# Kernel tuning notes

Measured on AMD Instinct MI355X. Metric: run time of the kernel, lower is better.

## Reference

```python
import jax, jax.numpy as jnp
import numpy as np
from math import factorial

D = 2          # qudit dimension
L = 13         # number of qudits: state dim = D**L = 8192
J, K = 0, 1    # levels coupled by the gate
CUTOFF = 10    # Taylor truncation order
INDEX = set(range(13))


def _series(z, parity):
    # sum_{i=1..CUTOFF, i%2==parity} z**i / i!   (truncated exp split into even/odd parts)
    s = jnp.zeros((), dtype=jnp.complex64)
    for i in range(1, CUTOFF + 1):
        if i % 2 == parity:
            s = s + z ** i / factorial(i)
    return s


def _gate(theta):
    # single-qudit RX gate matrix, truncated-Taylor version matching the torch code
    z = (-0.5j) * theta.astype(jnp.complex64)
    odd = _series(z, 1)   # ~ -i sin(theta/2)
    even = _series(z, 0)  # ~ cos(theta/2) - 1
    M = jnp.eye(D, dtype=jnp.complex64)
    M = M.at[J, K].add(odd)
    M = M.at[K, J].add(odd)
    M = M.at[J, J].add(even)
    M = M.at[K, K].add(even)
    return M


def setup_inputs() -> dict:
    key = jax.random.key(0)
    k1, k2, k3 = jax.random.split(key, 3)
    dim = D ** L
    return {
        "x_real": jax.random.normal(k1, (dim, 64), dtype=jnp.float32),
        "x_imag": jax.random.normal(k2, (dim, 64), dtype=jnp.float32),
        "angle": jax.random.normal(k3, (L,), dtype=jnp.float32),
    }


def reference(x_real, x_imag, angle):
    x = x_real.astype(jnp.complex64) + 1j * x_imag.astype(jnp.complex64)
    eye = jnp.eye(D, dtype=jnp.complex64)
    U = jnp.eye(1, dtype=jnp.complex64)
    for i in range(L):  # fixed structural loop over qudits (13 iterations)
        M = _gate(angle[i]) if i in INDEX else eye
        U = jnp.kron(U, M)
    out = U @ x  # [D^L, B] complex64
    return jnp.stack([out.real, out.imag])  # [2, D^L, B] float32
```

## Files before the change

### kernel.cpp

```cpp
#include <hip/hip_runtime.h>

#define PLANE (8192 * 64)

__device__ __forceinline__ void gate_coeffs(float theta, float& a, float& s) {
    float t = 0.5f * theta;
    float u = t * t;
    s = t * (1.f + u * (-1.f/6.f + u * (1.f/120.f + u * (-1.f/5040.f + u * (1.f/362880.f)))));
    a = 1.f + u * (-0.5f + u * (1.f/24.f + u * (-1.f/720.f + u * (1.f/40320.f + u * (-1.f/3628800.f)))));
}

__device__ __forceinline__ void butterfly(float4& v0, float4& v1, float a, float s) {
    float4 n0, n1;
    n0.x = a * v0.x + s * v1.y;
    n0.y = a * v0.y - s * v1.x;
    n0.z = a * v0.z + s * v1.w;
    n0.w = a * v0.w - s * v1.z;
    n1.x = a * v1.x + s * v0.y;
    n1.y = a * v1.y - s * v0.x;
    n1.z = a * v1.z + s * v0.w;
    n1.w = a * v1.w - s * v0.z;
    v0 = n0; v1 = n1;
}

__global__ __launch_bounds__(256) void rx_low(const float* __restrict__ xr,
                                              const float* __restrict__ xi,
                                              const float* __restrict__ angle,
                                              float4* __restrict__ ws4) {
    __shared__ float4 l4[64 * 8];
    const int tid = threadIdx.x;
    const int g   = blockIdx.x >> 2;
    const int q   = blockIdx.x & 3;

    const float4* xr4 = (const float4*)xr;
    const float4* xi4 = (const float4*)xi;

    {
        int lr = tid >> 2, c4 = tid & 3;
        int ga = (g * 64 + lr) * 16 + q * 4 + c4;
        float4 re = xr4[ga];
        float4 im = xi4[ga];
        l4[lr * 8 + c4 * 2]     = make_float4(re.x, im.x, re.y, im.y);
        l4[lr * 8 + c4 * 2 + 1] = make_float4(re.z, im.z, re.w, im.w);
    }
    __syncthreads();

    #pragma unroll
    for (int b = 0; b < 6; ++b) {
        float a, s;
        gate_coeffs(angle[12 - b], a, s);
        int cp = tid & 7, rp = tid >> 3;
        int lo = ((rp >> b) << (b + 1)) | (rp & ((1 << b) - 1));
        int i0 = lo * 8 + cp;
        int i1 = i0 + (8 << b);
        float4 v0 = l4[i0], v1 = l4[i1];
        butterfly(v0, v1, a, s);
        l4[i0] = v0; l4[i1] = v1;
        __syncthreads();
    }

    #pragma unroll
    for (int k = 0; k < 2; ++k) {
        int j = tid + 256 * k;
        int m = j >> 3, cp = j & 7;
        ws4[(q * 8192 + m * 128 + g) * 8 + cp] = l4[j];
    }
}

__global__ __launch_bounds__(256) void rx_high(const float* __restrict__ angle,
                                               const float4* __restrict__ ws4,
                                               float* __restrict__ out) {
    __shared__ float4 l4[128 * 8];
    const int tid = threadIdx.x;
    const int g   = blockIdx.x >> 2;
    const int q   = blockIdx.x & 3;

    const float4* src = ws4 + (size_t)(q * 8192 + g * 128) * 8;
    typedef const __attribute__((address_space(1))) unsigned int* g32;
    typedef __attribute__((address_space(3))) unsigned int* l32;
    #pragma unroll
    for (int k = 0; k < 4; ++k) {
        int j = tid + 256 * k;
        __builtin_amdgcn_global_load_lds((g32)(src + j), (l32)(l4 + j), 16, 0, 0);
    }
    asm volatile("s_waitcnt vmcnt(0)" ::: "memory");
    __syncthreads();

    #pragma unroll
    for (int qq = 0; qq < 7; ++qq) {
        float a, s;
        gate_coeffs(angle[6 - qq], a, s);
        #pragma unroll
        for (int pp = 0; pp < 2; ++pp) {
            int p  = tid + 256 * pp;
            int cp = p & 7, hp = p >> 3;
            int h0 = ((hp >> qq) << (qq + 1)) | (hp & ((1 << qq) - 1));
            int i0 = h0 * 8 + cp;
            int i1 = i0 + (8 << qq);
            float4 v0 = l4[i0], v1 = l4[i1];
            butterfly(v0, v1, a, s);
            l4[i0] = v0; l4[i1] = v1;
        }
        __syncthreads();
    }

    float2* outre2 = (float2*)out;
    float2* outim2 = (float2*)(out + PLANE);
    #pragma unroll
    for (int k = 0; k < 4; ++k) {
        int j = tid + 256 * k;
        int h = j >> 3, cp = j & 7;
        float4 v = l4[j];
        int r  = g + 64 * h;
        int o2 = r * 32 + q * 8 + cp;
        outre2[o2] = make_float2(v.x, v.z);
        outim2[o2] = make_float2(v.y, v.w);
    }
}

extern "C" void kernel_launch(void* const* d_in, const int* in_sizes, int n_in,
                              void* d_out, int out_size, void* d_ws, size_t ws_size,
                              hipStream_t stream) {
    const float* xr    = (const float*)d_in[0];
    const float* xi    = (const float*)d_in[1];
    const float* angle = (const float*)d_in[2];
    float*  out = (float*)d_out;
    float4* ws4 = (float4*)d_ws;

    rx_low<<<512, 256, 0, stream>>>(xr, xi, angle, ws4);
    rx_high<<<256, 256, 0, stream>>>(angle, ws4, out);
}
```

Baseline: 14.20 us.

## Fuse butterfly stages in registers, swizzle LDS, and retile high kernel

Each thread now does two qubit stages per LDS round trip (a radix-4 step over four rows held in registers). This halves the number of shared-memory passes and barriers. Both kernels use XOR-swizzled LDS indexing to avoid bank conflicts, and gate coefficients are computed up front. Blocks shrink to 128 threads, and the workspace layout is retiled so rx_high uses 512 blocks and writes float4 output rows instead of float2. The swizzled intermediate layout adds index arithmetic and must agree exactly between the two kernels.

```diff
diff --git a/kernel.cpp b/kernel.cpp
--- a/kernel.cpp
+++ b/kernel.cpp
@@ -9,111 +9,184 @@
     a = 1.f + u * (-0.5f + u * (1.f/24.f + u * (-1.f/720.f + u * (1.f/40320.f + u * (-1.f/3628800.f)))));
 }
 
-__device__ __forceinline__ void butterfly(float4& v0, float4& v1, float a, float s) {
+__device__ __forceinline__ void bf(float4& v0, float4& v1, float a, float s) {
     float4 n0, n1;
-    n0.x = a * v0.x + s * v1.y;
-    n0.y = a * v0.y - s * v1.x;
-    n0.z = a * v0.z + s * v1.w;
-    n0.w = a * v0.w - s * v1.z;
-    n1.x = a * v1.x + s * v0.y;
-    n1.y = a * v1.y - s * v0.x;
-    n1.z = a * v1.z + s * v0.w;
-    n1.w = a * v1.w - s * v0.z;
+    n0.x = a * v0.x + s * v1.y;  n0.y = a * v0.y - s * v1.x;
+    n0.z = a * v0.z + s * v1.w;  n0.w = a * v0.w - s * v1.z;
+    n1.x = a * v1.x + s * v0.y;  n1.y = a * v1.y - s * v0.x;
+    n1.z = a * v1.z + s * v0.w;  n1.w = a * v1.w - s * v0.z;
     v0 = n0; v1 = n1;
 }
 
-__global__ __launch_bounds__(256) void rx_low(const float* __restrict__ xr,
+__device__ __forceinline__ int swzA(int row, int cp) {
+    return row * 8 + (cp ^ ((row ^ (row >> 3)) & 7));
+}
+__device__ __forceinline__ int sB(int h) { return (h ^ (h >> 2) ^ (h >> 4)) & 3; }
+__device__ __forceinline__ int swzB(int h, int cp) {
+    return h * 4 + (cp ^ sB(h));
+}
+
+__global__ __launch_bounds__(128) void rx_low(const float* __restrict__ xr,
                                               const float* __restrict__ xi,
                                               const float* __restrict__ angle,
                                               float4* __restrict__ ws4) {
-    __shared__ float4 l4[64 * 8];
-    const int tid = threadIdx.x;
-    const int g   = blockIdx.x >> 2;
-    const int q   = blockIdx.x & 3;
+    __shared__ float4 la[512];
+    const int t  = threadIdx.x;
+    const int g  = blockIdx.x >> 2;
+    const int qq = blockIdx.x & 3;
+
+    float a0,s0,a1,s1,a2,s2,a3,s3,a4,s4,a5,s5;
+    gate_coeffs(angle[12], a0, s0);
+    gate_coeffs(angle[11], a1, s1);
+    gate_coeffs(angle[10], a2, s2);
+    gate_coeffs(angle[9],  a3, s3);
+    gate_coeffs(angle[8],  a4, s4);
+    gate_coeffs(angle[7],  a5, s5);
 
     const float4* xr4 = (const float4*)xr;
     const float4* xi4 = (const float4*)xi;
 
-    {
-        int lr = tid >> 2, c4 = tid & 3;
-        int ga = (g * 64 + lr) * 16 + q * 4 + c4;
-        float4 re = xr4[ga];
-        float4 im = xi4[ga];
-        l4[lr * 8 + c4 * 2]     = make_float4(re.x, im.x, re.y, im.y);
-        l4[lr * 8 + c4 * 2 + 1] = make_float4(re.z, im.z, re.w, im.w);
-    }
-    __syncthreads();
-
-    #pragma unroll
-    for (int b = 0; b < 6; ++b) {
-        float a, s;
-        gate_coeffs(angle[12 - b], a, s);
-        int cp = tid & 7, rp = tid >> 3;
-        int lo = ((rp >> b) << (b + 1)) | (rp & ((1 << b) - 1));
-        int i0 = lo * 8 + cp;
-        int i1 = i0 + (8 << b);
-        float4 v0 = l4[i0], v1 = l4[i1];
-        butterfly(v0, v1, a, s);
-        l4[i0] = v0; l4[i1] = v1;
-        __syncthreads();
-    }
-
     #pragma unroll
     for (int k = 0; k < 2; ++k) {
-        int j = tid + 256 * k;
-        int m = j >> 3, cp = j & 7;
-        ws4[(q * 8192 + m * 128 + g) * 8 + cp] = l4[j];
-    }
-}
-
-__global__ __launch_bounds__(256) void rx_high(const float* __restrict__ angle,
+        int j   = t + 128 * k;
+        int row = j >> 2, f4 = j & 3;
+        int ga  = (g * 64 + row) * 16 + qq * 4 + f4;
+        float4 re = xr4[ga], im = xi4[ga];
+        la[swzA(row, 2 * f4)]     = make_float4(re.x, im.x, re.y, im.y);
+        la[swzA(row, 2 * f4 + 1)] = make_float4(re.z, im.z, re.w, im.w);
+    }
+    __syncthreads();
+
+    const int cp = t & 7, grp = t >> 3;
+
+    {
+        int r0 = grp * 4;
+        float4 v0 = la[swzA(r0 + 0, cp)], v1 = la[swzA(r0 + 1, cp)];
+        float4 v2 = la[swzA(r0 + 2, cp)], v3 = la[swzA(r0 + 3, cp)];
+        bf(v0, v1, a0, s0); bf(v2, v3, a0, s0);
+        bf(v0, v2, a1, s1); bf(v1, v3, a1, s1);
+        la[swzA(r0 + 0, cp)] = v0; la[swzA(r0 + 1, cp)] = v1;
+        la[swzA(r0 + 2, cp)] = v2; la[swzA(r0 + 3, cp)] = v3;
+    }
+    __syncthreads();
+    {
+        int base = ((grp >> 2) << 4) | (grp & 3);
+        int r0 = base, r1 = base + 4, r2 = base + 8, r3 = base + 12;
+        float4 v0 = la[swzA(r0, cp)], v1 = la[swzA(r1, cp)];
+        float4 v2 = la[swzA(r2, cp)], v3 = la[swzA(r3, cp)];
+        bf(v0, v1, a2, s2); bf(v2, v3, a2, s2);
+        bf(v0, v2, a3, s3); bf(v1, v3, a3, s3);
+        la[swzA(r0, cp)] = v0; la[swzA(r1, cp)] = v1;
+        la[swzA(r2, cp)] = v2; la[swzA(r3, cp)] = v3;
+    }
+    __syncthreads();
+    {
+        int r0 = grp, r1 = grp + 16, r2 = grp + 32, r3 = grp + 48;
+        float4 v0 = la[swzA(r0, cp)], v1 = la[swzA(r1, cp)];
+        float4 v2 = la[swzA(r2, cp)], v3 = la[swzA(r3, cp)];
+        bf(v0, v1, a4, s4); bf(v2, v3, a4, s4);
+        bf(v0, v2, a5, s5); bf(v1, v3, a5, s5);
+        la[swzA(r0, cp)] = v0; la[swzA(r1, cp)] = v1;
+        la[swzA(r2, cp)] = v2; la[swzA(r3, cp)] = v3;
+    }
+    __syncthreads();
+
+    const int sbg = sB(g);
+    #pragma unroll
+    for (int k = 0; k < 4; ++k) {
+        int j  = t + 128 * k;
+        int m  = j >> 3, cp8 = j & 7;
+        int q  = qq * 2 + (cp8 >> 2), cb = cp8 & 3;
+        ws4[(q * 64 + m) * 512 + g * 4 + (cb ^ sbg)] = la[swzA(m, cp8)];
+    }
+}
+
+__global__ __launch_bounds__(128) void rx_high(const float* __restrict__ angle,
                                                const float4* __restrict__ ws4,
                                                float* __restrict__ out) {
-    __shared__ float4 l4[128 * 8];
-    const int tid = threadIdx.x;
-    const int g   = blockIdx.x >> 2;
-    const int q   = blockIdx.x & 3;
-
-    const float4* src = ws4 + (size_t)(q * 8192 + g * 128) * 8;
+    __shared__ float4 lb[512];
+    const int t = threadIdx.x;
+    const int m = blockIdx.x >> 3;
+    const int q = blockIdx.x & 7;
+
+    float a0,s0,a1,s1,a2,s2,a3,s3,a4,s4,a5,s5,a6,s6;
+    gate_coeffs(angle[6], a0, s0);
+    gate_coeffs(angle[5], a1, s1);
+    gate_coeffs(angle[4], a2, s2);
+    gate_coeffs(angle[3], a3, s3);
+    gate_coeffs(angle[2], a4, s4);
+    gate_coeffs(angle[1], a5, s5);
+    gate_coeffs(angle[0], a6, s6);
+
+    const float4* src = ws4 + (size_t)(q * 64 + m) * 512;
     typedef const __attribute__((address_space(1))) unsigned int* g32;
     typedef __attribute__((address_space(3))) unsigned int* l32;
     #pragma unroll
     for (int k = 0; k < 4; ++k) {
-        int j = tid + 256 * k;
-        __builtin_amdgcn_global_load_lds((g32)(src + j), (l32)(l4 + j), 16, 0, 0);
+        int slot = t + 128 * k;
+        __builtin_amdgcn_global_load_lds((g32)(src + slot), (l32)(lb + slot), 16, 0, 0);
     }
     asm volatile("s_waitcnt vmcnt(0)" ::: "memory");
     __syncthreads();
 
-    #pragma unroll
-    for (int qq = 0; qq < 7; ++qq) {
-        float a, s;
-        gate_coeffs(angle[6 - qq], a, s);
+    const int cp = t & 3, grp = t >> 2;
+
+    {
+        int h0 = grp * 4;
+        float4 v0 = lb[swzB(h0 + 0, cp)], v1 = lb[swzB(h0 + 1, cp)];
+        float4 v2 = lb[swzB(h0 + 2, cp)], v3 = lb[swzB(h0 + 3, cp)];
+        bf(v0, v1, a0, s0); bf(v2, v3, a0, s0);
+        bf(v0, v2, a1, s1); bf(v1, v3, a1, s1);
+        lb[swzB(h0 + 0, cp)] = v0; lb[swzB(h0 + 1, cp)] = v1;
+        lb[swzB(h0 + 2, cp)] = v2; lb[swzB(h0 + 3, cp)] = v3;
+    }
+    __syncthreads();
+    {
+        int base = ((grp >> 2) << 4) | (grp & 3);
+        int h0 = base, h1 = base + 4, h2 = base + 8, h3 = base + 12;
+        float4 v0 = lb[swzB(h0, cp)], v1 = lb[swzB(h1, cp)];
+        float4 v2 = lb[swzB(h2, cp)], v3 = lb[swzB(h3, cp)];
+        bf(v0, v1, a2, s2); bf(v2, v3, a2, s2);
+        bf(v0, v2, a3, s3); bf(v1, v3, a3, s3);
+        lb[swzB(h0, cp)] = v0; lb[swzB(h1, cp)] = v1;
+        lb[swzB(h2, cp)] = v2; lb[swzB(h3, cp)] = v3;
+    }
+    __syncthreads();
+    {
+        int base = ((grp >> 4) << 6) | (grp & 15);
+        int h0 = base, h1 = base + 16, h2 = base + 32, h3 = base + 48;
+        float4 v0 = lb[swzB(h0, cp)], v1 = lb[swzB(h1, cp)];
+        float4 v2 = lb[swzB(h2, cp)], v3 = lb[swzB(h3, cp)];
+        bf(v0, v1, a4, s4); bf(v2, v3, a4, s4);
+        bf(v0, v2, a5, s5); bf(v1, v3, a5, s5);
+        lb[swzB(h0, cp)] = v0; lb[swzB(h1, cp)] = v1;
+        lb[swzB(h2, cp)] = v2; lb[swzB(h3, cp)] = v3;
+    }
+    __syncthreads();
+    {
         #pragma unroll
         for (int pp = 0; pp < 2; ++pp) {
-            int p  = tid + 256 * pp;
-            int cp = p & 7, hp = p >> 3;
-            int h0 = ((hp >> qq) << (qq + 1)) | (hp & ((1 << qq) - 1));
-            int i0 = h0 * 8 + cp;
-            int i1 = i0 + (8 << qq);
-            float4 v0 = l4[i0], v1 = l4[i1];
-            butterfly(v0, v1, a, s);
-            l4[i0] = v0; l4[i1] = v1;
+            int p  = t + 128 * pp;
+            int cpP = p & 3, hl = p >> 2;
+            float4 v0 = lb[swzB(hl, cpP)], v1 = lb[swzB(hl + 64, cpP)];
+            bf(v0, v1, a6, s6);
+            lb[swzB(hl, cpP)] = v0; lb[swzB(hl + 64, cpP)] = v1;
         }
-        __syncthreads();
-    }
-
-    float2* outre2 = (float2*)out;
-    float2* outim2 = (float2*)(out + PLANE);
+    }
+    __syncthreads();
+
+    float4* or4 = (float4*)out;
+    float4* oi4 = (float4*)(out + PLANE);
     #pragma unroll
     for (int k = 0; k < 4; ++k) {
-        int j = tid + 256 * k;
-        int h = j >> 3, cp = j & 7;
-        float4 v = l4[j];
-        int r  = g + 64 * h;
-        int o2 = r * 32 + q * 8 + cp;
-        outre2[o2] = make_float2(v.x, v.z);
-        outim2[o2] = make_float2(v.y, v.w);
+        int j   = t + 128 * k;
+        int h   = j >> 2, pl = (j >> 1) & 1, f4c = j & 1;
+        float4 v0 = lb[swzB(h, f4c * 2)];
+        float4 v1 = lb[swzB(h, f4c * 2 + 1)];
+        float4 val = pl ? make_float4(v0.y, v0.w, v1.y, v1.w)
+                        : make_float4(v0.x, v0.z, v1.x, v1.z);
+        float4* dst = pl ? oi4 : or4;
+        dst[((h << 6) | m) * 16 + q * 2 + f4c] = val;
     }
 }
 
@@ -126,6 +199,6 @@
     float*  out = (float*)d_out;
     float4* ws4 = (float4*)d_ws;
 
-    rx_low<<<512, 256, 0, stream>>>(xr, xi, angle, ws4);
-    rx_high<<<256, 256, 0, stream>>>(angle, ws4, out);
-}
+    rx_low<<<512, 128, 0, stream>>>(xr, xi, angle, ws4);
+    rx_high<<<512, 128, 0, stream>>>(angle, ws4, out);
+}
```

After: 15.76 us. 10.9% more time.
